# Performance work log

Measured on AMD Instinct MI355X. Metric: run time of the kernel, lower is better.

Reference implementation:

```python
import jax, jax.numpy as jnp
import numpy as np

N = 100000   # nodes
E = 1600000  # edges (avg degree 16)
IN = 128     # in_channels
H = 256      # hidden_channels
L = 3        # num_layers
C = 2        # num_classes
EPS = 1e-5   # BatchNorm eps


def setup_inputs() -> dict:
    key = jax.random.key(0)
    ks = jax.random.split(key, 8)
    s = 0.05
    x = jax.random.normal(ks[0], (N, IN), jnp.float32)
    edge_index = jax.random.randint(ks[1], (2, E), 0, N)
    return dict(
        x=x,
        edge_index=edge_index,
        proj_w=jax.random.normal(ks[2], (IN, H), jnp.float32) * s,
        proj_b=jnp.zeros((H,), jnp.float32),
        lin_l_w=jax.random.normal(ks[3], (L, H, H), jnp.float32) * s,
        lin_l_b=jnp.zeros((L, H), jnp.float32),
        lin_r_w=jax.random.normal(ks[4], (L, H, H), jnp.float32) * s,
        bn_g=jnp.ones((L, H), jnp.float32),
        bn_b=jnp.zeros((L, H), jnp.float32),
        fc1_w=jax.random.normal(ks[5], (H, H // 2), jnp.float32) * s,
        fc1_b=jnp.zeros((H // 2,), jnp.float32),
        fc2_w=jax.random.normal(ks[6], (H // 2, C), jnp.float32) * s,
        fc2_b=jnp.zeros((C,), jnp.float32),
    )


def reference(x, edge_index, proj_w, proj_b, lin_l_w, lin_l_b, lin_r_w,
              bn_g, bn_b, fc1_w, fc1_b, fc2_w, fc2_b):
    src, dst = edge_index[0], edge_index[1]
    # in-degree for mean aggregation (SAGEConv aggr='mean')
    deg = jax.ops.segment_sum(jnp.ones((E,), x.dtype), dst, num_segments=N)
    inv_deg = (1.0 / jnp.maximum(deg, 1.0))[:, None]  # [N,1]

    h = jax.nn.relu(x @ proj_w + proj_b)  # [N,H]; dropout is identity in eval
    for i in range(L):
        # SAGEConv: lin_l(mean_{j in N(i)} h_j) + lin_r(h_i)
        agg = jax.ops.segment_sum(h[src], dst, num_segments=N) * inv_deg  # [N,H]
        out = agg @ lin_l_w[i] + lin_l_b[i] + h @ lin_r_w[i]
        # BatchNorm over nodes (batch statistics, biased variance)
        mu = out.mean(axis=0)
        var = out.var(axis=0)
        out = (out - mu) * jax.lax.rsqrt(var + EPS) * bn_g[i] + bn_b[i]
        out = jax.nn.relu(out)
        h = out + h if i > 0 else out  # residual from layer 1 onward

    embeddings = h
    z = jax.nn.relu(embeddings @ fc1_w + fc1_b)
    logits = z @ fc2_w + fc2_b
    return (logits, embeddings)
```

## Files before the change

### kernel.cpp

```cpp
#include <hip/hip_runtime.h>
#include <stdint.h>

#define NN 100000
#define NE 1600000
#define INC 128
#define HID 256
#define MP  100096
#define NBK 391
#define EPB 2048

typedef unsigned short u16;
typedef __attribute__((ext_vector_type(2))) float f32x2;
typedef __attribute__((ext_vector_type(4))) float f32x4;
typedef __attribute__((ext_vector_type(8))) short s16x8;

static __device__ __forceinline__ float bf2f(u16 u){
  union { uint32_t i; float f; } v; v.i = ((uint32_t)u) << 16; return v.f;
}
static __device__ __forceinline__ u16 f2bf(float f){
  union { float f; uint32_t i; } v; v.f = f;
  uint32_t r = v.i + 0x7FFFu + ((v.i >> 16) & 1u);
  return (u16)(r >> 16);
}
static __device__ __forceinline__ void up8(uint4 o, float* v){
  v[0]=bf2f((u16)(o.x&0xffffu)); v[1]=bf2f((u16)(o.x>>16));
  v[2]=bf2f((u16)(o.y&0xffffu)); v[3]=bf2f((u16)(o.y>>16));
  v[4]=bf2f((u16)(o.z&0xffffu)); v[5]=bf2f((u16)(o.z>>16));
  v[6]=bf2f((u16)(o.w&0xffffu)); v[7]=bf2f((u16)(o.w>>16));
}
static __device__ __forceinline__ uint4 pk8(const float* v){
  uint4 o;
  o.x = (uint32_t)f2bf(v[0]) | ((uint32_t)f2bf(v[1])<<16);
  o.y = (uint32_t)f2bf(v[2]) | ((uint32_t)f2bf(v[3])<<16);
  o.z = (uint32_t)f2bf(v[4]) | ((uint32_t)f2bf(v[5])<<16);
  o.w = (uint32_t)f2bf(v[6]) | ((uint32_t)f2bf(v[7])<<16);
  return o;
}
static __device__ __forceinline__ uint2 pkf8(const float* r){
  uint32_t lo = __builtin_amdgcn_cvt_pk_fp8_f32(r[0], r[1], 0u, false);
  lo = __builtin_amdgcn_cvt_pk_fp8_f32(r[2], r[3], lo, true);
  uint32_t hi = __builtin_amdgcn_cvt_pk_fp8_f32(r[4], r[5], 0u, false);
  hi = __builtin_amdgcn_cvt_pk_fp8_f32(r[6], r[7], hi, true);
  return make_uint2(lo, hi);
}

static __device__ __forceinline__ void gload16(const void* g, void* l){
  __builtin_amdgcn_global_load_lds((const __attribute__((address_space(1))) void*)g,
                                   (__attribute__((address_space(3))) void*)l, 16, 0, 0);
}


__global__ __launch_bounds__(256) void zero_k(float* bnacc, int* bcnt){
  int i = blockIdx.x*256 + threadIdx.x;
  if (i < 3*8192) bnacc[i] = 0.f;
  if (i < NBK) bcnt[i] = 0;
}

__global__ __launch_bounds__(256) void cvt_k(const float* __restrict__ src, u16* __restrict__ dst, int n4){
  int i = blockIdx.x*256 + threadIdx.x;
  if (i >= n4) return;
  float4 v = ((const float4*)src)[i];
  uint2 o;
  o.x = (uint32_t)f2bf(v.x) | ((uint32_t)f2bf(v.y)<<16);
  o.y = (uint32_t)f2bf(v.z) | ((uint32_t)f2bf(v.w)<<16);
  ((uint2*)dst)[i] = o;
}

__global__ __launch_bounds__(256) void cvt8_k(const uint4* __restrict__ h, uint2* __restrict__ h8, int n){
  int i = blockIdx.x*256 + threadIdx.x;
  if (i >= n) return;
  float v[8];
  up8(h[i], v);
  h8[i] = pkf8(v);
}

__global__ __launch_bounds__(256) void pack_k(const float* __restrict__ src, u16* __restrict__ dst,
                                              int K, int NC, int ksoff){
  int t = blockIdx.x*256 + threadIdx.x;
  if (t >= K*NC) return;
  int k = t / NC, n = t % NC;
  int NT = NC >> 4;
  int ks = ksoff + (k >> 5);
  int l  = ((k >> 3) & 3)*16 + (n & 15);
  int j  = k & 7;
  dst[((size_t)(ks*NT + (n>>4))*64 + l)*8 + j] = f2bf(src[(size_t)k*NC + n]);
}


__global__ __launch_bounds__(256) void bhist_k(const int* __restrict__ ei, int* __restrict__ bcnt){
  __shared__ int h[NBK];
  for (int i = threadIdx.x; i < NBK; i += 256) h[i] = 0;
  __syncthreads();
  int e0 = blockIdx.x * EPB;
  #pragma unroll
  for (int j = 0; j < EPB/256; ++j){
    int e = e0 + j*256 + threadIdx.x;
    if (e < NE) atomicAdd(&h[ei[NE + e] >> 8], 1);
  }
  __syncthreads();
  for (int i = threadIdx.x; i < NBK; i += 256)
    if (h[i]) atomicAdd(&bcnt[i], h[i]);
}

__global__ __launch_bounds__(512) void bscan_k(const int* __restrict__ bcnt, int* __restrict__ bcur){
  __shared__ int sd[512];
  int t = threadIdx.x;
  int v = (t < NBK) ? bcnt[t] : 0;
  sd[t] = v; __syncthreads();
  for (int o = 1; o < 512; o <<= 1){
    int x = (t >= o) ? sd[t-o] : 0;
    __syncthreads();
    sd[t] += x;
    __syncthreads();
  }
  if (t < NBK) bcur[t] = sd[t] - v;
}

__global__ __launch_bounds__(256) void bfill_k(const int* __restrict__ ei, int* __restrict__ bcur,
                                               unsigned* __restrict__ epair){
  __shared__ int cnt[NBK];
  __shared__ int gb[NBK];
  for (int i = threadIdx.x; i < NBK; i += 256) cnt[i] = 0;
  __syncthreads();
  int e0 = blockIdx.x * EPB;
  unsigned pk[EPB/256];
  int bkt[EPB/256], rnk[EPB/256];
  #pragma unroll
  for (int j = 0; j < EPB/256; ++j){
    int e = e0 + j*256 + threadIdx.x;
    if (e < NE){
      int s = ei[e];
      int d = ei[NE + e];
      bkt[j] = d >> 8;
      pk[j]  = ((unsigned)s << 8) | (unsigned)(d & 255);
      rnk[j] = atomicAdd(&cnt[bkt[j]], 1);
    } else bkt[j] = -1;
  }
  __syncthreads();
  for (int i = threadIdx.x; i < NBK; i += 256){
    int c = cnt[i];
    gb[i] = c ? atomicAdd(&bcur[i], c) : 0;
  }
  __syncthreads();
  #pragma unroll
  for (int j = 0; j < EPB/256; ++j){
    if (bkt[j] >= 0)
      epair[gb[bkt[j]] + rnk[j]] = pk[j];
  }
}

__global__ __launch_bounds__(256) void csort_k(const unsigned* __restrict__ epair,
                                               const int* __restrict__ bcnt, const int* __restrict__ bcur,
                                               int* __restrict__ ci, int* __restrict__ rp){
  __shared__ int hist[256], pfx[256], cnt2[256];
  int b = blockIdx.x, t = threadIdx.x;
  int cnt  = bcnt[b];
  int base = bcur[b] - cnt;
  hist[t] = 0; cnt2[t] = 0;
  __syncthreads();
  for (int e = t; e < cnt; e += 256)
    atomicAdd(&hist[epair[base + e] & 255u], 1);
  __syncthreads();
  int v = hist[t];
  pfx[t] = v;
  __syncthreads();
  for (int o = 1; o < 256; o <<= 1){
    int x = (t >= o) ? pfx[t - o] : 0;
    __syncthreads();
    pfx[t] += x;
    __syncthreads();
  }
  int node = b*256 + t;
  if (node < NN) rp[node] = base + pfx[t] - v;
  if (b == NBK-1 && t == 0) rp[NN] = NE;
  for (int e = t; e < cnt; e += 256){
    unsigned p = epair[base + e];
    int ld = (int)(p & 255u);
    int r  = atomicAdd(&cnt2[ld], 1);
    ci[base + pfx[ld] - hist[ld] + r] = (int)(p >> 8);
  }
}


__global__ __launch_bounds__(256) void agg8_k(const int* __restrict__ rp, const int* __restrict__ ci,
                                              const uint4* __restrict__ h8, u16* __restrict__ ag){
  int wid  = (int)((blockIdx.x*256u + threadIdx.x) >> 6);
  int lane = threadIdx.x & 63;
  int ql   = lane & 15;
  int w    = wid*4 + (lane >> 4);
  bool act = (w < NN);
  int e0 = 0, e1 = 0;
  if (act){ e0 = rp[w]; e1 = rp[w+1]; }
  int cnt = e1 - e0;

  float a[16];
  #pragma unroll
  for (int k = 0; k < 16; ++k) a[k] = 0.f;

  for (int base = 0; __any(base < cnt); base += 16){
    int rem = cnt - base;
    int my = 0;
    if (ql < rem) my = ci[e0 + base + ql];
    #pragma unroll
    for (int j0 = 0; j0 < 16; j0 += 8){
      if (!__any(j0 < rem)) break;
      uint4 v[8];
      #pragma unroll
      for (int jj = 0; jj < 8; ++jj){
        int j = j0 + jj;
        int s = __shfl(my, (lane & 48) + j);
        v[jj] = make_uint4(0,0,0,0);
        if (j < rem) v[jj] = h8[(size_t)s*16 + ql];
      }
      #pragma unroll
      for (int jj = 0; jj < 8; ++jj){
        uint32_t wd[4] = {v[jj].x, v[jj].y, v[jj].z, v[jj].w};
        #pragma unroll
        for (int p = 0; p < 4; ++p){
          f32x2 lo = __builtin_amdgcn_cvt_pk_f32_fp8(wd[p], false);
          f32x2 hi = __builtin_amdgcn_cvt_pk_f32_fp8(wd[p], true);
          a[p*4+0] += lo[0]; a[p*4+1] += lo[1];
          a[p*4+2] += hi[0]; a[p*4+3] += hi[1];
        }
      }
    }
  }

  if (act){
    float inv = 1.0f / (float)(cnt > 0 ? cnt : 1);
    float r0[8], r1[8];
    #pragma unroll
    for (int k = 0; k < 8; ++k){ r0[k] = a[k]*inv; r1[k] = a[8+k]*inv; }
    uint4* agu = (uint4*)ag;
    agu[(size_t)w*32 + ql*2]     = pk8(r0);
    agu[(size_t)w*32 + ql*2 + 1] = pk8(r1);
  }
}


__global__ __launch_bounds__(256) void aggb_k(const int* __restrict__ rp, const int* __restrict__ ci,
                                              const u16* __restrict__ h, u16* __restrict__ ag){
  int w = (int)((blockIdx.x*256u + threadIdx.x) >> 6);
  int lane = threadIdx.x & 63;
  if (w >= NN) return;
  int e0 = rp[w], e1 = rp[w+1];
  const uint2* hu = (const uint2*)h;
  float a0=0.f, a1=0.f, a2=0.f, a3=0.f;
  for (int base = e0; base < e1; base += 64){
    int cnt = e1 - base; if (cnt > 64) cnt = 64;
    int my = ci[base + (lane < cnt ? lane : cnt-1)];
    int i = 0;
    for (; i + 8 <= cnt; i += 8){
      int s[8];
      #pragma unroll
      for (int jj = 0; jj < 8; ++jj) s[jj] = __builtin_amdgcn_readlane(my, i + jj);
      uint2 v[8];
      #pragma unroll
      for (int jj = 0; jj < 8; ++jj) v[jj] = hu[(size_t)s[jj]*64 + lane];
      #pragma unroll
      for (int jj = 0; jj < 8; ++jj){
        a0 += bf2f((u16)(v[jj].x & 0xffffu));
        a1 += bf2f((u16)(v[jj].x >> 16));
        a2 += bf2f((u16)(v[jj].y & 0xffffu));
        a3 += bf2f((u16)(v[jj].y >> 16));
      }
    }
    for (; i < cnt; ++i){
      int s0 = __builtin_amdgcn_readlane(my, i);
      uint2 v = hu[(size_t)s0*64 + lane];
      a0 += bf2f((u16)(v.x&0xffffu));
      a1 += bf2f((u16)(v.x>>16));
      a2 += bf2f((u16)(v.y&0xffffu));
      a3 += bf2f((u16)(v.y>>16));
    }
  }
  int d = e1 - e0;
  float inv = 1.0f / (float)(d > 0 ? d : 1);
  uint2 o;
  o.x = (uint32_t)f2bf(a0*inv) | ((uint32_t)f2bf(a1*inv) << 16);
  o.y = (uint32_t)f2bf(a2*inv) | ((uint32_t)f2bf(a3*inv) << 16);
  ((uint2*)ag)[(size_t)w*64 + lane] = o;
}


template<int KS1, int KS2, int NCC, int EPI>
__global__ __launch_bounds__(256, 3) void gemm3_k(
    const u16* __restrict__ A1, const u16* __restrict__ A2,
    const u16* __restrict__ Wp, const float* __restrict__ bias,
    u16* __restrict__ Cout, int M, float* __restrict__ stS)
{
  constexpr int NT    = NCC >> 4;
  constexpr int NFRAG = NCC / 64;
  constexpr int NS1   = KS1 / 2;
  constexpr int NSTEP = (KS1 + KS2) / 2;

  __shared__ u16 Al[2][64*64];

  const int t    = threadIdx.x;
  const int lane = t & 63;
  const int wv   = t >> 6;
  const int r15  = lane & 15, kg = lane >> 4;
  const int rb   = blockIdx.x * 64;
  const int nt0w = wv * NFRAG;

  f32x4 acc[4][NFRAG];
  #pragma unroll
  for (int m = 0; m < 4; ++m)
    #pragma unroll
    for (int n = 0; n < NFRAG; ++n){ f32x4 z = {0.f,0.f,0.f,0.f}; acc[m][n] = z; }

  auto stageA = [&](int step, int bsel){
    const bool inA1 = (step < NS1);
    const u16* Ab   = inA1 ? A1 : A2;
    const int  Krow = (inA1 ? KS1 : KS2) * 32;
    const int  kloc = (inA1 ? step : step - NS1) * 64;
    #pragma unroll
    for (int c = 0; c < 2; ++c){
      int row = c*32 + wv*8 + (lane >> 3);
      int gc  = (lane & 7) ^ (row & 7);
      const u16* g = Ab + (size_t)(rb + row)*Krow + kloc + gc*8;
      gload16(g, &Al[bsel][c*2048 + wv*512]);
    }
  };
  auto loadB = [&](int ss, s16x8* dst){
    const u16* g = Wp + ((size_t)(ss*NT + nt0w)*64 + lane)*8;
    #pragma unroll
    for (int n = 0; n < NFRAG; ++n)
      dst[n] = *(const s16x8*)(g + (size_t)n*512);
  };

  s16x8 bb[2][NFRAG];
  stageA(0, 0);
  loadB(0, bb[0]);
  __syncthreads();

  #pragma unroll
  for (int step = 0; step < NSTEP; ++step){
    const int cur = step & 1;
    if (step + 1 < NSTEP) stageA(step + 1, cur ^ 1);
    #pragma unroll
    for (int sl = 0; sl < 2; ++sl){
      const int ss = step*2 + sl;
      const int p  = ss & 1;
      if (ss + 1 < NSTEP*2) loadB(ss + 1, bb[p ^ 1]);
      s16x8 af[4];
      const char* Ab = (const char*)&Al[cur][0];
      #pragma unroll
      for (int m = 0; m < 4; ++m){
        int row = m*16 + r15;
        int c16 = (sl*4 + kg) ^ (row & 7);
        af[m] = *(const s16x8*)(Ab + row*128 + c16*16);
      }
      #pragma unroll
      for (int m = 0; m < 4; ++m)
        #pragma unroll
        for (int n = 0; n < NFRAG; ++n)
          acc[m][n] = __builtin_amdgcn_mfma_f32_16x16x32_bf16(af[m], bb[p][n], acc[m][n], 0, 0, 0);
    }
    __syncthreads();
  }

  #pragma unroll
  for (int n = 0; n < NFRAG; ++n){
    int col = (nt0w + n)*16 + r15;
    float bc = bias[col];
    float s = 0.f, q = 0.f;
    #pragma unroll
    for (int m = 0; m < 4; ++m){
      int rbase = rb + m*16 + kg*4;
      #pragma unroll
      for (int r = 0; r < 4; ++r){
        int row = rbase + r;
        float val = acc[m][n][r] + bc;
        if (EPI == 0) val = fmaxf(val, 0.f);
        bool ok = row < M;
        if (ok) Cout[(size_t)row*NCC + col] = f2bf(val);
        if (EPI == 1 && ok){ s += val; q += val*val; }
      }
    }
    if (EPI == 1){
      s += __shfl_xor(s, 16); s += __shfl_xor(s, 32);
      q += __shfl_xor(q, 16); q += __shfl_xor(q, 32);
      if (lane < 16){
        int idx = ((blockIdx.x & 15) << 9) + col;
        atomicAdd(&stS[idx], s);
        atomicAdd(&stS[idx + 256], q);
      }
    }
  }
}


__global__ __launch_bounds__(256) void bnfin_k(const float* __restrict__ acc,
                                               const float* __restrict__ g, const float* __restrict__ b,
                                               float* __restrict__ coef){
  int c = threadIdx.x;
  float s = 0.f, q = 0.f;
  #pragma unroll
  for (int j = 0; j < 16; ++j){
    s += acc[j*512 + c];
    q += acc[j*512 + 256 + c];
  }
  float mean = s * (1.0f / (float)NN);
  float var  = q * (1.0f / (float)NN) - mean*mean;
  float sc = g[c] * rsqrtf(var + 1e-5f);
  coef[c] = sc;
  coef[256 + c] = b[c] - mean*sc;
}

__global__ __launch_bounds__(256) void bnapply_k(const uint4* __restrict__ outb, uint4* __restrict__ h,
                                                 uint2* __restrict__ h8,
                                                 const float* __restrict__ coef, int layer, int wr8,
                                                 float* __restrict__ embout){
  int i = blockIdx.x*256 + threadIdx.x;
  if (i >= NN*32) return;
  int col0 = (i & 31) * 8;
  const float4* scp = (const float4*)(coef + col0);
  const float4* shp = (const float4*)(coef + 256 + col0);
  float4 s0 = scp[0], s1 = scp[1], t0 = shp[0], t1 = shp[1];
  float sc[8] = {s0.x,s0.y,s0.z,s0.w,s1.x,s1.y,s1.z,s1.w};
  float sh[8] = {t0.x,t0.y,t0.z,t0.w,t1.x,t1.y,t1.z,t1.w};
  float v[8], r[8];
  up8(outb[i], v);
  #pragma unroll
  for (int j = 0; j < 8; ++j) r[j] = fmaxf(v[j]*sc[j] + sh[j], 0.f);
  if (layer > 0){
    float hv[8];
    up8(h[i], hv);
    #pragma unroll
    for (int j = 0; j < 8; ++j) r[j] += hv[j];
  }
  h[i] = pk8(r);
  if (wr8) h8[i] = pkf8(r);
  if (embout){
    int row = i >> 5;
    float4* ep = (float4*)(embout + (size_t)row*256 + col0);
    ep[0] = make_float4(r[0], r[1], r[2], r[3]);
    ep[1] = make_float4(r[4], r[5], r[6], r[7]);
  }
}


__global__ __launch_bounds__(256) void fc2_k(const u16* __restrict__ z, const float* __restrict__ w2,
                                             const float* __restrict__ b2, float* __restrict__ out){
  int w = (int)((blockIdx.x*256u + threadIdx.x) >> 6);
  int lane = threadIdx.x & 63;
  if (w >= NN) return;
  const uint32_t* zu = (const uint32_t*)(z + (size_t)w*128);
  uint32_t p = zu[lane];
  float z0 = bf2f((u16)(p & 0xffffu));
  float z1 = bf2f((u16)(p >> 16));
  float4 wv = ((const float4*)w2)[lane];
  float p0 = z0*wv.x + z1*wv.z;
  float p1 = z0*wv.y + z1*wv.w;
  #pragma unroll
  for (int off = 1; off < 64; off <<= 1){
    p0 += __shfl_xor(p0, off);
    p1 += __shfl_xor(p1, off);
  }
  if (lane == 0){
    out[(size_t)w*2]     = p0 + b2[0];
    out[(size_t)w*2 + 1] = p1 + b2[1];
  }
}


extern "C" void kernel_launch(void* const* d_in, const int* in_sizes, int n_in,
                              void* d_out, int out_size, void* d_ws, size_t ws_size,
                              hipStream_t stream){
  const float* x       = (const float*)d_in[0];
  const int*   ei      = (const int*)d_in[1];
  const float* proj_w  = (const float*)d_in[2];
  const float* proj_b  = (const float*)d_in[3];
  const float* lin_l_w = (const float*)d_in[4];
  const float* lin_l_b = (const float*)d_in[5];
  const float* lin_r_w = (const float*)d_in[6];
  const float* bn_g    = (const float*)d_in[7];
  const float* bn_b    = (const float*)d_in[8];
  const float* fc1_w   = (const float*)d_in[9];
  const float* fc1_b   = (const float*)d_in[10];
  const float* fc2_w   = (const float*)d_in[11];
  const float* fc2_b   = (const float*)d_in[12];
  float* out = (float*)d_out;

  char* ws = (char*)d_ws;
  size_t off = 0;
  auto alloc = [&](size_t b){ size_t o = off; off = (off + b + 255) & ~(size_t)255; return o; };

  u16* bufA    = (u16*)(ws + alloc((size_t)MP*256*2));
  u16* hbuf    = (u16*)(ws + alloc((size_t)MP*256*2));
  u16* bufC    = (u16*)(ws + alloc((size_t)MP*256*2));
  uint8_t* h8  = (uint8_t*)(ws + alloc((size_t)MP*256));
  u16* wp_proj = (u16*)(ws + alloc((size_t)4*16*64*8*2));
  u16* wp_l[3];
  for (int i = 0; i < 3; ++i) wp_l[i] = (u16*)(ws + alloc((size_t)16*16*64*8*2));
  u16* wp_fc1  = (u16*)(ws + alloc((size_t)8*8*64*8*2));
  int* rp    = (int*)(ws + alloc((size_t)(NN+1)*4));
  int* ci    = (int*)(ws + alloc((size_t)NE*4));
  int* bcnt  = (int*)(ws + alloc(NBK*4));
  int* bcur  = (int*)(ws + alloc(NBK*4));
  float* bnacc = (float*)(ws + alloc(3*8192*4));
  float* coef  = (float*)(ws + alloc(3*512*4));
  unsigned* epair = (unsigned*)bufC;
  (void)ws_size; (void)in_sizes; (void)n_in; (void)out_size;

  const int BFB = (NE + EPB - 1)/EPB;
  const int GX = MP/64;

  zero_k<<<96, 256, 0, stream>>>(bnacc, bcnt);

  bhist_k<<<BFB, 256, 0, stream>>>(ei, bcnt);
  bscan_k<<<1, 512, 0, stream>>>(bcnt, bcur);
  bfill_k<<<BFB, 256, 0, stream>>>(ei, bcur, epair);
  csort_k<<<NBK, 256, 0, stream>>>(epair, bcnt, bcur, ci, rp);

  cvt_k<<<(NN*INC/4 + 255)/256, 256, 0, stream>>>(x, bufA, NN*INC/4);
  pack_k<<<(128*256 + 255)/256, 256, 0, stream>>>(proj_w, wp_proj, 128, 256, 0);
  for (int i = 0; i < 3; ++i){
    pack_k<<<(256*256 + 255)/256, 256, 0, stream>>>(lin_l_w + (size_t)i*65536, wp_l[i], 256, 256, 0);
    pack_k<<<(256*256 + 255)/256, 256, 0, stream>>>(lin_r_w + (size_t)i*65536, wp_l[i], 256, 256, 8);
  }
  pack_k<<<(256*128 + 255)/256, 256, 0, stream>>>(fc1_w, wp_fc1, 256, 128, 0);

  gemm3_k<4,0,256,0><<<GX, 256, 0, stream>>>(bufA, nullptr, wp_proj, proj_b,
                                             hbuf, NN, nullptr);
  cvt8_k<<<(NN*32 + 255)/256, 256, 0, stream>>>((const uint4*)hbuf, (uint2*)h8, NN*32);

  for (int i = 0; i < 3; ++i){
    if (i < 2)
      agg8_k<<<((NN + 3)/4*64 + 255)/256, 256, 0, stream>>>(rp, ci, (const uint4*)h8, bufA);
    else
      aggb_k<<<(NN + 3)/4, 256, 0, stream>>>(rp, ci, hbuf, bufA);
    gemm3_k<8,8,256,1><<<GX, 256, 0, stream>>>(bufA, hbuf, wp_l[i], lin_l_b + (size_t)i*256,
                                               bufC, NN, bnacc + i*8192);
    bnfin_k<<<1, 256, 0, stream>>>(bnacc + i*8192, bn_g + (size_t)i*256, bn_b + (size_t)i*256, coef + i*512);
    bnapply_k<<<(NN*32 + 255)/256, 256, 0, stream>>>((const uint4*)bufC, (uint4*)hbuf, (uint2*)h8,
                                                     coef + i*512, i, (i == 0) ? 1 : 0,
                                                     (i == 2) ? (out + 200000) : nullptr);
  }

  gemm3_k<8,0,128,0><<<GX, 256, 0, stream>>>(hbuf, nullptr, wp_fc1, fc1_b,
                                             bufA, NN, nullptr);
  fc2_k<<<(NN + 3)/4, 256, 0, stream>>>(bufA, fc2_w, fc2_b, out);
}
```

Before: 689.1 us.

## Fuse fc2 into fc1 GEMM epilogue and merge prep kernels into one launch

The fc1 GEMM gains an epilogue mode that applies bias and ReLU, then takes the dot product with the two fc2 weight columns and reduces it across lanes and waves through shared memory. Logits are written directly, so the intermediate z buffer is neither stored nor read back. Separately, the input conversion, the weight packing launches and the zeroing kernel are merged into one block-dispatched prep kernel to cut launch overhead. The extra shared-memory reduction array in the GEMM template could slightly affect occupancy for the other instantiations.

New measurement: 646.4 us (median of 2 runs). 6.2% less time.

```diff
diff --git a/kernel.cpp b/kernel.cpp
--- a/kernel.cpp
+++ b/kernel.cpp
@@ -49,41 +49,56 @@
                                    (__attribute__((address_space(3))) void*)l, 16, 0, 0);
 }
 
-
-__global__ __launch_bounds__(256) void zero_k(float* bnacc, int* bcnt){
-  int i = blockIdx.x*256 + threadIdx.x;
-  if (i < 3*8192) bnacc[i] = 0.f;
-  if (i < NBK) bcnt[i] = 0;
-}
-
-__global__ __launch_bounds__(256) void cvt_k(const float* __restrict__ src, u16* __restrict__ dst, int n4){
-  int i = blockIdx.x*256 + threadIdx.x;
-  if (i >= n4) return;
-  float4 v = ((const float4*)src)[i];
-  uint2 o;
-  o.x = (uint32_t)f2bf(v.x) | ((uint32_t)f2bf(v.y)<<16);
-  o.y = (uint32_t)f2bf(v.z) | ((uint32_t)f2bf(v.w)<<16);
-  ((uint2*)dst)[i] = o;
-}
-
-__global__ __launch_bounds__(256) void cvt8_k(const uint4* __restrict__ h, uint2* __restrict__ h8, int n){
-  int i = blockIdx.x*256 + threadIdx.x;
-  if (i >= n) return;
-  float v[8];
-  up8(h[i], v);
-  h8[i] = pkf8(v);
-}
-
-__global__ __launch_bounds__(256) void pack_k(const float* __restrict__ src, u16* __restrict__ dst,
-                                              int K, int NC, int ksoff){
-  int t = blockIdx.x*256 + threadIdx.x;
-  if (t >= K*NC) return;
+static __device__ __forceinline__ void packw(const float* __restrict__ src, u16* __restrict__ dst,
+                                             int K, int NC, int ksoff, int t){
   int k = t / NC, n = t % NC;
   int NT = NC >> 4;
   int ks = ksoff + (k >> 5);
   int l  = ((k >> 3) & 3)*16 + (n & 15);
   int j  = k & 7;
   dst[((size_t)(ks*NT + (n>>4))*64 + l)*8 + j] = f2bf(src[(size_t)k*NC + n]);
+}
+
+
+__global__ __launch_bounds__(256) void prep_k(
+    const float* __restrict__ x, u16* __restrict__ xbf,
+    const float* __restrict__ proj_w, u16* __restrict__ wp_proj,
+    const float* __restrict__ lin_l_w, const float* __restrict__ lin_r_w,
+    u16* __restrict__ wp_l0, u16* __restrict__ wp_l1, u16* __restrict__ wp_l2,
+    const float* __restrict__ fc1_w, u16* __restrict__ wp_fc1,
+    float* __restrict__ bnacc, int* __restrict__ bcnt)
+{
+  int b = blockIdx.x;
+  int tid = threadIdx.x;
+  if (b < 12500){
+    int i = b*256 + tid;
+    float4 v = ((const float4*)x)[i];
+    uint2 o;
+    o.x = (uint32_t)f2bf(v.x) | ((uint32_t)f2bf(v.y)<<16);
+    o.y = (uint32_t)f2bf(v.z) | ((uint32_t)f2bf(v.w)<<16);
+    ((uint2*)xbf)[i] = o;
+    return;
+  }
+  b -= 12500;
+  if (b < 128){ packw(proj_w, wp_proj, 128, 256, 0, b*256 + tid); return; }
+  b -= 128;
+  if (b < 1536){
+    int wsel = b >> 8;
+    int t = (b & 255)*256 + tid;
+    int i = wsel >> 1;
+    u16* dst = (i == 0) ? wp_l0 : (i == 1) ? wp_l1 : wp_l2;
+    if (wsel & 1) packw(lin_r_w + (size_t)i*65536, dst, 256, 256, 8, t);
+    else          packw(lin_l_w + (size_t)i*65536, dst, 256, 256, 0, t);
+    return;
+  }
+  b -= 1536;
+  if (b < 128){ packw(fc1_w, wp_fc1, 256, 128, 0, b*256 + tid); return; }
+  b -= 128;
+  {
+    int i = b*256 + tid;
+    if (i < 3*8192) bnacc[i] = 0.f;
+    if (i < NBK) bcnt[i] = 0;
+  }
 }
 
 
@@ -287,7 +302,8 @@
 __global__ __launch_bounds__(256, 3) void gemm3_k(
     const u16* __restrict__ A1, const u16* __restrict__ A2,
     const u16* __restrict__ Wp, const float* __restrict__ bias,
-    u16* __restrict__ Cout, int M, float* __restrict__ stS)
+    u16* __restrict__ Cout, int M, float* __restrict__ stS,
+    const float* __restrict__ w2, const float* __restrict__ b2, float* __restrict__ out2)
 {
   constexpr int NT    = NCC >> 4;
   constexpr int NFRAG = NCC / 64;
@@ -295,6 +311,7 @@
   constexpr int NSTEP = (KS1 + KS2) / 2;
 
   __shared__ u16 Al[2][64*64];
+  __shared__ float red[4][64][2];
 
   const int t    = threadIdx.x;
   const int lane = t & 63;
@@ -358,6 +375,53 @@
           acc[m][n] = __builtin_amdgcn_mfma_f32_16x16x32_bf16(af[m], bb[p][n], acc[m][n], 0, 0, 0);
     }
     __syncthreads();
+  }
+
+  if (EPI == 2){
+    float p[4][4][2];
+    #pragma unroll
+    for (int m = 0; m < 4; ++m)
+      #pragma unroll
+      for (int r = 0; r < 4; ++r){ p[m][r][0] = 0.f; p[m][r][1] = 0.f; }
+    #pragma unroll
+    for (int n = 0; n < NFRAG; ++n){
+      int col = (nt0w + n)*16 + r15;
+      float bc = bias[col];
+      float w0 = w2[col*2], w1 = w2[col*2 + 1];
+      #pragma unroll
+      for (int m = 0; m < 4; ++m)
+        #pragma unroll
+        for (int r = 0; r < 4; ++r){
+          float val = fmaxf(acc[m][n][r] + bc, 0.f);
+          p[m][r][0] += val*w0;
+          p[m][r][1] += val*w1;
+        }
+    }
+    #pragma unroll
+    for (int off = 1; off < 16; off <<= 1)
+      #pragma unroll
+      for (int m = 0; m < 4; ++m)
+        #pragma unroll
+        for (int r = 0; r < 4; ++r){
+          p[m][r][0] += __shfl_xor(p[m][r][0], off);
+          p[m][r][1] += __shfl_xor(p[m][r][1], off);
+        }
+    if (r15 == 0){
+      #pragma unroll
+      for (int m = 0; m < 4; ++m)
+        #pragma unroll
+        for (int r = 0; r < 4; ++r){
+          red[wv][m*16 + kg*4 + r][0] = p[m][r][0];
+          red[wv][m*16 + kg*4 + r][1] = p[m][r][1];
+        }
+    }
+    __syncthreads();
+    if (t < 128){
+      int row = t >> 1, c = t & 1;
+      float s = red[0][row][c] + red[1][row][c] + red[2][row][c] + red[3][row][c] + b2[c];
+      if (rb + row < M) out2[(size_t)(rb + row)*2 + c] = s;
+    }
+    return;
   }
 
   #pragma unroll
@@ -440,28 +504,12 @@
   }
 }
 
-
-__global__ __launch_bounds__(256) void fc2_k(const u16* __restrict__ z, const float* __restrict__ w2,
-                                             const float* __restrict__ b2, float* __restrict__ out){
-  int w = (int)((blockIdx.x*256u + threadIdx.x) >> 6);
-  int lane = threadIdx.x & 63;
-  if (w >= NN) return;
-  const uint32_t* zu = (const uint32_t*)(z + (size_t)w*128);
-  uint32_t p = zu[lane];
-  float z0 = bf2f((u16)(p & 0xffffu));
-  float z1 = bf2f((u16)(p >> 16));
-  float4 wv = ((const float4*)w2)[lane];
-  float p0 = z0*wv.x + z1*wv.z;
-  float p1 = z0*wv.y + z1*wv.w;
-  #pragma unroll
-  for (int off = 1; off < 64; off <<= 1){
-    p0 += __shfl_xor(p0, off);
-    p1 += __shfl_xor(p1, off);
-  }
-  if (lane == 0){
-    out[(size_t)w*2]     = p0 + b2[0];
-    out[(size_t)w*2 + 1] = p1 + b2[1];
-  }
+__global__ __launch_bounds__(256) void cvt8_k(const uint4* __restrict__ h, uint2* __restrict__ h8, int n){
+  int i = blockIdx.x*256 + threadIdx.x;
+  if (i >= n) return;
+  float v[8];
+  up8(h[i], v);
+  h8[i] = pkf8(v);
 }
 
 
@@ -506,24 +554,18 @@
 
   const int BFB = (NE + EPB - 1)/EPB;
   const int GX = MP/64;
-
-  zero_k<<<96, 256, 0, stream>>>(bnacc, bcnt);
+  const int PREPB = 12500 + 128 + 1536 + 128 + 96;
+
+  prep_k<<<PREPB, 256, 0, stream>>>(x, bufA, proj_w, wp_proj, lin_l_w, lin_r_w,
+                                    wp_l[0], wp_l[1], wp_l[2], fc1_w, wp_fc1, bnacc, bcnt);
 
   bhist_k<<<BFB, 256, 0, stream>>>(ei, bcnt);
   bscan_k<<<1, 512, 0, stream>>>(bcnt, bcur);
   bfill_k<<<BFB, 256, 0, stream>>>(ei, bcur, epair);
   csort_k<<<NBK, 256, 0, stream>>>(epair, bcnt, bcur, ci, rp);
 
-  cvt_k<<<(NN*INC/4 + 255)/256, 256, 0, stream>>>(x, bufA, NN*INC/4);
-  pack_k<<<(128*256 + 255)/256, 256, 0, stream>>>(proj_w, wp_proj, 128, 256, 0);
-  for (int i = 0; i < 3; ++i){
-    pack_k<<<(256*256 + 255)/256, 256, 0, stream>>>(lin_l_w + (size_t)i*65536, wp_l[i], 256, 256, 0);
-    pack_k<<<(256*256 + 255)/256, 256, 0, stream>>>(lin_r_w + (size_t)i*65536, wp_l[i], 256, 256, 8);
-  }
-  pack_k<<<(256*128 + 255)/256, 256, 0, stream>>>(fc1_w, wp_fc1, 256, 128, 0);
-
   gemm3_k<4,0,256,0><<<GX, 256, 0, stream>>>(bufA, nullptr, wp_proj, proj_b,
-                                             hbuf, NN, nullptr);
+                                             hbuf, NN, nullptr, nullptr, nullptr, nullptr);
   cvt8_k<<<(NN*32 + 255)/256, 256, 0, stream>>>((const uint4*)hbuf, (uint2*)h8, NN*32);
 
   for (int i = 0; i < 3; ++i){
@@ -532,14 +574,13 @@
     else
       aggb_k<<<(NN + 3)/4, 256, 0, stream>>>(rp, ci, hbuf, bufA);
     gemm3_k<8,8,256,1><<<GX, 256, 0, stream>>>(bufA, hbuf, wp_l[i], lin_l_b + (size_t)i*256,
-                                               bufC, NN, bnacc + i*8192);
+                                               bufC, NN, bnacc + i*8192, nullptr, nullptr, nullptr);
     bnfin_k<<<1, 256, 0, stream>>>(bnacc + i*8192, bn_g + (size_t)i*256, bn_b + (size_t)i*256, coef + i*512);
     bnapply_k<<<(NN*32 + 255)/256, 256, 0, stream>>>((const uint4*)bufC, (uint4*)hbuf, (uint2*)h8,
                                                      coef + i*512, i, (i == 0) ? 1 : 0,
                                                      (i == 2) ? (out + 200000) : nullptr);
   }
 
-  gemm3_k<8,0,128,0><<<GX, 256, 0, stream>>>(hbuf, nullptr, wp_fc1, fc1_b,
-                                             bufA, NN, nullptr);
-  fc2_k<<<(NN + 3)/4, 256, 0, stream>>>(bufA, fc2_w, fc2_b, out);
-}
+  gemm3_k<8,0,128,2><<<GX, 256, 0, stream>>>(hbuf, nullptr, wp_fc1, fc1_b,
+                                             nullptr, NN, nullptr, fc2_w, fc2_b, out);
+}
```
